# Kernel optimization log

Measured on AMD Instinct MI355X. Metric: run time of the kernel, lower is better.

The kernel has to match this reference:

```python
import jax, jax.numpy as jnp
import numpy as np

B, S, H = 8, 1024, 768
NH, DH = 12, 64
F, E = 3072, 8
EPS = 1e-12

def layer_norm(x, g, b):
    mu = jnp.mean(x, axis=-1, keepdims=True)
    var = jnp.var(x, axis=-1, keepdims=True)
    return g * (x - mu) / jnp.sqrt(var + EPS) + b

def setup_inputs():
    key = jax.random.key(0)
    ks = jax.random.split(key, 20)
    std = 0.02
    d = {
        'hidden_states': jax.random.normal(ks[0], (B, S, H), jnp.float32),
        'Wq': jax.random.normal(ks[1], (H, H)) * std, 'bq': jnp.zeros((H,)),
        'Wk': jax.random.normal(ks[2], (H, H)) * std, 'bk': jnp.zeros((H,)),
        'Wv': jax.random.normal(ks[3], (H, H)) * std, 'bv': jnp.zeros((H,)),
        'Wao': jax.random.normal(ks[4], (H, H)) * std, 'bao': jnp.zeros((H,)),
        'ln1_g': jnp.ones((H,)), 'ln1_b': jnp.zeros((H,)),
        'Wr': jax.random.normal(ks[5], (H, E)) * std, 'br': jnp.zeros((E,)),
        'Wi': jax.random.normal(ks[6], (E, H, F)) * std, 'bi': jnp.zeros((E, F)),
        'Wo': jax.random.normal(ks[7], (F, H)) * std, 'bo': jnp.zeros((H,)),
        'ln2_g': jnp.ones((H,)), 'ln2_b': jnp.zeros((H,)),
    }
    return d

def reference(hidden_states, Wq, bq, Wk, bk, Wv, bv, Wao, bao, ln1_g, ln1_b,
              Wr, br, Wi, bi, Wo, bo, ln2_g, ln2_b):
    b, s, h = hidden_states.shape
    # --- self attention ---
    q = (hidden_states @ Wq + bq).reshape(b, s, NH, DH)
    k = (hidden_states @ Wk + bk).reshape(b, s, NH, DH)
    v = (hidden_states @ Wv + bv).reshape(b, s, NH, DH)
    scores = jnp.einsum('bqhd,bkhd->bhqk', q, k) / jnp.sqrt(jnp.float32(DH))
    probs = jax.nn.softmax(scores, axis=-1)
    ctx = jnp.einsum('bhqk,bkhd->bqhd', probs, v).reshape(b, s, h)
    attention_output = layer_norm(ctx @ Wao + bao + hidden_states, ln1_g, ln1_b)
    # --- router ---
    routing_scores = jax.nn.softmax(attention_output @ Wr + br, axis=-1)  # [b,s,E]
    routing_expert = jnp.argmax(routing_scores, axis=-1)  # [b,s]
    # --- expert FFN (dispatch/combine via per-expert masking) ---
    flat_x = attention_output.reshape(-1, h)          # [T,H]
    flat_e = routing_expert.reshape(-1)               # [T]
    flat_inter = jnp.zeros((b * s, F), flat_x.dtype)
    for e in range(E):
        mask = (flat_e == e)[:, None].astype(flat_x.dtype)
        y = jax.nn.gelu(flat_x @ Wi[e] + bi[e], approximate=False)
        flat_inter = flat_inter + mask * y
    inter = flat_inter.reshape(b, s, F)
    # --- output (dense + residual layernorm) ---
    layer_output = layer_norm(inter @ Wo + bo + attention_output, ln2_g, ln2_b)
    return layer_output, routing_scores
```

## Files before the change

kernel.cpp:

```cpp
#include <hip/hip_runtime.h>
#include <math.h>
#include <stdint.h>

#define TOKS 8192
#define HDIM 768
#define FDIM 3072
#define NEXP 8
#define NHEAD 12
#define SEQ 1024
#define BATCH 8
#define PERMSZ 9216

typedef __attribute__((ext_vector_type(8))) short s16x8;
typedef __attribute__((ext_vector_type(4))) short s16x4;
typedef __attribute__((ext_vector_type(4))) float f32x4;

__device__ __forceinline__ short f2bf(float f) {
  uint32_t u = __float_as_uint(f);
  uint32_t r = (u + 0x7fffu + ((u >> 16) & 1u)) >> 16;
  return (short)(r & 0xffffu);
}
__device__ __forceinline__ float bf2f(short h) {
  return __uint_as_float(((uint32_t)(uint16_t)h) << 16);
}
__device__ __forceinline__ void gload16(const void* g, void* l) {
  __builtin_amdgcn_global_load_lds(
      (const __attribute__((address_space(1))) uint32_t*)g,
      (__attribute__((address_space(3))) uint32_t*)l, 16, 0, 0);
}
__device__ __forceinline__ void pipe_wait_barrier() {
  asm volatile("s_waitcnt vmcnt(0)" ::: "memory");
  __builtin_amdgcn_s_barrier();
}

__global__ __launch_bounds__(256) void convert_split(
    const float* __restrict__ X, short* __restrict__ Xh, short* __restrict__ Xl, int n4)
{
  const int i = blockIdx.x * 256 + threadIdx.x;
  if (i >= n4) return;
  const float4 v = ((const float4*)X)[i];
  const float a[4] = {v.x, v.y, v.z, v.w};
  s16x4 h, l;
#pragma unroll
  for (int j = 0; j < 4; ++j) {
    h[j] = f2bf(a[j]);
    l[j] = f2bf(a[j] - bf2f(h[j]));
  }
  ((s16x4*)Xh)[i] = h;
  ((s16x4*)Xl)[i] = l;
}

__global__ __launch_bounds__(256) void transpose_split(
    const float* __restrict__ W, short* __restrict__ WTh, short* __restrict__ WTl,
    int K, int N)
{
  __shared__ float t[32][33];
  const int tid = threadIdx.x;
  const int tx = tid & 31, ty = tid >> 5;
  const int n0 = blockIdx.x * 32, k0 = blockIdx.y * 32;
#pragma unroll
  for (int r = 0; r < 4; ++r)
    t[ty + r * 8][tx] = W[(size_t)(k0 + ty + r * 8) * N + n0 + tx];
  __syncthreads();
#pragma unroll
  for (int r = 0; r < 4; ++r) {
    const float v = t[tx][ty + r * 8];
    const short h = f2bf(v);
    WTh[(size_t)(n0 + ty + r * 8) * K + k0 + tx] = h;
    WTl[(size_t)(n0 + ty + r * 8) * K + k0 + tx] = f2bf(v - bf2f(h));
  }
}

__global__ __launch_bounds__(256) void qkv_split_mfma(
    const short* __restrict__ Ah, const short* __restrict__ Al,
    const short* __restrict__ BhT, const short* __restrict__ BlT,
    const float* __restrict__ bias,
    short* __restrict__ QKh, short* __restrict__ QKl,
    short* __restrict__ VTh, short* __restrict__ VTl)
{
  const int K = 768;
  __shared__ __align__(16) short lAh[4096];
  __shared__ __align__(16) short lAl[4096];
  __shared__ __align__(16) short lBh[2][4096];
  __shared__ __align__(16) short lBl[2][4096];
  const int dsp = blockIdx.x + 18 * blockIdx.y;
  const int orig = (dsp & 7) * 144 + (dsp >> 3);
  const int bx = orig % 18, by = orig / 18;
  const int tid = threadIdx.x;
  const int w = tid >> 6, lane = tid & 63;
  const int wr = w >> 1, wc = w & 1;
  const int row0 = by * 128, col0 = bx * 128;
  const int sr = lane & 15, kg = lane >> 4;
  const size_t a0 = (size_t)(row0 + 2 * w * 16 + sr) * K + kg * 8;
  const size_t a1 = a0 + (size_t)16 * K;
  const size_t b0 = (size_t)(col0 + 2 * w * 16 + sr) * K + kg * 8;
  const size_t b1 = b0 + (size_t)16 * K;
  const int d0 = (2 * w) * 512, d1 = (2 * w + 1) * 512;
#define STAGE_QA(k0) do { \
    gload16(Ah + a0 + (k0), &lAh[d0]); \
    gload16(Ah + a1 + (k0), &lAh[d1]); \
    gload16(Al + a0 + (k0), &lAl[d0]); \
    gload16(Al + a1 + (k0), &lAl[d1]); \
  } while (0)
#define STAGE_QB(bu, k0) do { \
    gload16(BhT + b0 + (k0), &lBh[bu][d0]); \
    gload16(BhT + b1 + (k0), &lBh[bu][d1]); \
    gload16(BlT + b0 + (k0), &lBl[bu][d0]); \
    gload16(BlT + b1 + (k0), &lBl[bu][d1]); \
  } while (0)
  f32x4 acc[4][4] = {};
  STAGE_QA(0);
  STAGE_QB(0, 0);
  pipe_wait_barrier();
  int cur = 0;
  for (int t = 0; t < 24; ++t) {
    s16x8 ah[4], al[4], bh[4], bl[4];
#pragma unroll
    for (int i = 0; i < 4; ++i) {
      ah[i] = *(const s16x8*)&lAh[(wr * 4 + i) * 512 + lane * 8];
      al[i] = *(const s16x8*)&lAl[(wr * 4 + i) * 512 + lane * 8];
      bh[i] = *(const s16x8*)&lBh[cur][(wc * 4 + i) * 512 + lane * 8];
      bl[i] = *(const s16x8*)&lBl[cur][(wc * 4 + i) * 512 + lane * 8];
    }
    __syncthreads();
    if (t < 23) {
      STAGE_QA((t + 1) * 32);
      STAGE_QB(cur ^ 1, (t + 1) * 32);
    }
#pragma unroll
    for (int mi = 0; mi < 4; ++mi)
#pragma unroll
      for (int ni = 0; ni < 4; ++ni) {
        acc[mi][ni] = __builtin_amdgcn_mfma_f32_16x16x32_bf16(ah[mi], bh[ni], acc[mi][ni], 0, 0, 0);
        acc[mi][ni] = __builtin_amdgcn_mfma_f32_16x16x32_bf16(ah[mi], bl[ni], acc[mi][ni], 0, 0, 0);
        acc[mi][ni] = __builtin_amdgcn_mfma_f32_16x16x32_bf16(al[mi], bh[ni], acc[mi][ni], 0, 0, 0);
      }
    pipe_wait_barrier();
    cur ^= 1;
  }
#undef STAGE_QA
#undef STAGE_QB
  const int cl = lane & 15, rg = lane >> 4;
#pragma unroll
  for (int mi = 0; mi < 4; ++mi)
#pragma unroll
    for (int ni = 0; ni < 4; ++ni) {
      const int c = col0 + wc * 64 + ni * 16 + cl;
      const int rowb = row0 + wr * 64 + mi * 16 + rg * 4;
      const float qscale = (c < 768) ? 0.125f : 1.0f;
      s16x4 hv, lv;
#pragma unroll
      for (int r = 0; r < 4; ++r) {
        const float v = (acc[mi][ni][r] + bias[c]) * qscale;
        const short hh = f2bf(v);
        hv[r] = hh;
        lv[r] = f2bf(v - bf2f(hh));
      }
      if (c < 1536) {
#pragma unroll
        for (int r = 0; r < 4; ++r) {
          QKh[(size_t)(rowb + r) * 1536 + c] = hv[r];
          QKl[(size_t)(rowb + r) * 1536 + c] = lv[r];
        }
      } else {
        const int dall = c - 1536;
        const size_t vi = (((size_t)((rowb >> 10) * NHEAD + (dall >> 6))) * 64 + (dall & 63)) * 1024
                          + (rowb & 1023);
        *(s16x4*)(VTh + vi) = hv;
        *(s16x4*)(VTl + vi) = lv;
      }
    }
}

__global__ __launch_bounds__(256) void gemm_splitk_staged(
    const short* __restrict__ Ah, const short* __restrict__ Al,
    const short* __restrict__ BhT, const short* __restrict__ BlT,
    const float* __restrict__ bias, float* __restrict__ C0, float* __restrict__ C1,
    int N, int K)
{
  __shared__ __align__(16) short lAh[2][4096];
  __shared__ __align__(16) short lAl[2][4096];
  __shared__ __align__(16) short lBh[2][4096];
  __shared__ __align__(16) short lBl[2][4096];
  const int tid = threadIdx.x;
  const int w = tid >> 6, lane = tid & 63;
  const int wr = w >> 1, wc = w & 1;
  const int row0 = blockIdx.y * 128, col0 = blockIdx.x * 128;
  const int z = blockIdx.z;
  const int Khalf = K >> 1, koff = z * Khalf;
  const int sr = lane & 15, kg = lane >> 4;
  const size_t a0 = (size_t)(row0 + 2 * w * 16 + sr) * K + koff + kg * 8;
  const size_t a1 = a0 + (size_t)16 * K;
  const size_t b0 = (size_t)(col0 + 2 * w * 16 + sr) * K + koff + kg * 8;
  const size_t b1 = b0 + (size_t)16 * K;
  const int d0 = (2 * w) * 512, d1 = (2 * w + 1) * 512;
#define STAGE_K4(bu, k0) do { \
    gload16(Ah + a0 + (k0), &lAh[bu][d0]); \
    gload16(Ah + a1 + (k0), &lAh[bu][d1]); \
    gload16(Al + a0 + (k0), &lAl[bu][d0]); \
    gload16(Al + a1 + (k0), &lAl[bu][d1]); \
    gload16(BhT + b0 + (k0), &lBh[bu][d0]); \
    gload16(BhT + b1 + (k0), &lBh[bu][d1]); \
    gload16(BlT + b0 + (k0), &lBl[bu][d0]); \
    gload16(BlT + b1 + (k0), &lBl[bu][d1]); \
  } while (0)
  f32x4 acc[4][4] = {};
  const int NT = Khalf >> 5;
  STAGE_K4(0, 0);
  pipe_wait_barrier();
  int cur = 0;
  for (int t = 0; t < NT; ++t) {
    if (t + 1 < NT) STAGE_K4(cur ^ 1, (t + 1) * 32);
    s16x8 ah[4], al[4], bh[4], bl[4];
#pragma unroll
    for (int i = 0; i < 4; ++i) {
      ah[i] = *(const s16x8*)&lAh[cur][(wr * 4 + i) * 512 + lane * 8];
      al[i] = *(const s16x8*)&lAl[cur][(wr * 4 + i) * 512 + lane * 8];
      bh[i] = *(const s16x8*)&lBh[cur][(wc * 4 + i) * 512 + lane * 8];
      bl[i] = *(const s16x8*)&lBl[cur][(wc * 4 + i) * 512 + lane * 8];
    }
#pragma unroll
    for (int mi = 0; mi < 4; ++mi)
#pragma unroll
      for (int ni = 0; ni < 4; ++ni) {
        acc[mi][ni] = __builtin_amdgcn_mfma_f32_16x16x32_bf16(ah[mi], bh[ni], acc[mi][ni], 0, 0, 0);
        acc[mi][ni] = __builtin_amdgcn_mfma_f32_16x16x32_bf16(ah[mi], bl[ni], acc[mi][ni], 0, 0, 0);
        acc[mi][ni] = __builtin_amdgcn_mfma_f32_16x16x32_bf16(al[mi], bh[ni], acc[mi][ni], 0, 0, 0);
      }
    pipe_wait_barrier();
    cur ^= 1;
  }
#undef STAGE_K4
  float* C = z ? C1 : C0;
  const int cl = lane & 15, rg = lane >> 4;
#pragma unroll
  for (int mi = 0; mi < 4; ++mi)
#pragma unroll
    for (int r = 0; r < 4; ++r) {
      const int row = row0 + wr * 64 + mi * 16 + rg * 4 + r;
#pragma unroll
      for (int ni = 0; ni < 4; ++ni) {
        const int c = col0 + wc * 64 + ni * 16 + cl;
        C[(size_t)row * N + c] = acc[mi][ni][r] + (z ? 0.f : bias[c]);
      }
    }
}

__global__ __launch_bounds__(128, 2) void attention_part(
    const short* __restrict__ QKh, const short* __restrict__ QKl,
    const short* __restrict__ VTh, const short* __restrict__ VTl,
    float* __restrict__ O0, float* __restrict__ O1,
    float2* __restrict__ ml0, float2* __restrict__ ml1)
{
  __shared__ __align__(16) short lPh[2][2560];
  const int tid = threadIdx.x;
  const int w = tid >> 6, lane = tid & 63;
  const int dsp = blockIdx.x + 32 * (blockIdx.y + 12 * blockIdx.z);
  const int orig = (dsp & 7) * 384 + (dsp >> 3);
  const int wx = orig & 31;
  const int b = orig / 384, h = (orig >> 5) % 12;
  const int z = wx & 1;
  const int q0 = (wx >> 1) * 64 + w * 32;
  const int kv0 = z * 512;
  const int sr = lane & 15, kg = lane >> 4;
  const int cl = sr, rg = kg;
  short* myPh = lPh[w];
  float* Op = z ? O1 : O0;
  float2* mlp = z ? ml1 : ml0;

  s16x8 qh[2][2], ql[2][2];
  {
    const size_t qbase = ((size_t)b * SEQ + q0 + sr) * 1536 + h * 64 + kg * 8;
#pragma unroll
    for (int mi = 0; mi < 2; ++mi)
#pragma unroll
      for (int ks = 0; ks < 2; ++ks) {
        const size_t o = qbase + (size_t)mi * (16 * 1536) + ks * 32;
        qh[mi][ks] = *(const s16x8*)(QKh + o);
        ql[mi][ks] = *(const s16x8*)(QKl + o);
      }
  }
  float m_run[2][4], l_run[2][4];
#pragma unroll
  for (int mi = 0; mi < 2; ++mi)
#pragma unroll
    for (int r = 0; r < 4; ++r) { m_run[mi][r] = -3.0e38f; l_run[mi][r] = 0.f; }
  f32x4 acc_o[2][4] = {};

  for (int kt = kv0; kt < kv0 + 512; kt += 64) {
    s16x8 kh[4][2], kl2[4][2];
    {
      const size_t kbase = ((size_t)b * SEQ + kt + sr) * 1536 + 768 + h * 64 + kg * 8;
#pragma unroll
      for (int ni = 0; ni < 4; ++ni)
#pragma unroll
        for (int ks = 0; ks < 2; ++ks) {
          const size_t o = kbase + (size_t)ni * (16 * 1536) + ks * 32;
          kh[ni][ks] = *(const s16x8*)(QKh + o);
          kl2[ni][ks] = *(const s16x8*)(QKl + o);
        }
    }
    f32x4 accs[2][4] = {};
    __builtin_amdgcn_s_setprio(1);
#pragma unroll
    for (int ks = 0; ks < 2; ++ks)
#pragma unroll
      for (int ni = 0; ni < 4; ++ni)
#pragma unroll
        for (int mi = 0; mi < 2; ++mi) {
          accs[mi][ni] = __builtin_amdgcn_mfma_f32_16x16x32_bf16(qh[mi][ks], kh[ni][ks], accs[mi][ni], 0, 0, 0);
          accs[mi][ni] = __builtin_amdgcn_mfma_f32_16x16x32_bf16(qh[mi][ks], kl2[ni][ks], accs[mi][ni], 0, 0, 0);
          accs[mi][ni] = __builtin_amdgcn_mfma_f32_16x16x32_bf16(ql[mi][ks], kh[ni][ks], accs[mi][ni], 0, 0, 0);
        }
    __builtin_amdgcn_s_setprio(0);
    s16x8 vh[4][2], vl2[4][2];
    {
      const size_t vbase = (((size_t)(b * NHEAD + h)) * 64 + sr) * 1024 + kt + kg * 8;
#pragma unroll
      for (int nd = 0; nd < 4; ++nd)
#pragma unroll
        for (int ks2 = 0; ks2 < 2; ++ks2) {
          const size_t o = vbase + (size_t)nd * (16 * 1024) + ks2 * 32;
          vh[nd][ks2] = *(const s16x8*)(VTh + o);
          vl2[nd][ks2] = *(const s16x8*)(VTl + o);
        }
    }
#pragma unroll
    for (int mi = 0; mi < 2; ++mi)
#pragma unroll
      for (int r = 0; r < 4; ++r) {
        float mx = fmaxf(fmaxf(accs[mi][0][r], accs[mi][1][r]),
                         fmaxf(accs[mi][2][r], accs[mi][3][r]));
        mx = fmaxf(mx, __shfl_xor(mx, 1));
        mx = fmaxf(mx, __shfl_xor(mx, 2));
        mx = fmaxf(mx, __shfl_xor(mx, 4));
        mx = fmaxf(mx, __shfl_xor(mx, 8));
        const float mn = fmaxf(m_run[mi][r], mx);
        const float c = __expf(m_run[mi][r] - mn);
        m_run[mi][r] = mn;
        l_run[mi][r] *= c;
#pragma unroll
        for (int nd = 0; nd < 4; ++nd) acc_o[mi][nd][r] *= c;
        float sum = 0.f;
#pragma unroll
        for (int ni = 0; ni < 4; ++ni) {
          const float p = __expf(accs[mi][ni][r] - mn);
          const short hh = f2bf(p);
          sum += bf2f(hh);
          const int idx = (mi * 2 + (ni >> 1)) * 640 + (rg * 4 + r) * 40 + (ni & 1) * 16 + cl;
          myPh[idx] = hh;
        }
        sum += __shfl_xor(sum, 1);
        sum += __shfl_xor(sum, 2);
        sum += __shfl_xor(sum, 4);
        sum += __shfl_xor(sum, 8);
        l_run[mi][r] += sum;
      }
    __builtin_amdgcn_s_setprio(1);
#pragma unroll
    for (int ks2 = 0; ks2 < 2; ++ks2) {
      s16x8 pf[2];
#pragma unroll
      for (int mi = 0; mi < 2; ++mi) {
        const int ra = (mi * 2 + ks2) * 640 + sr * 40 + kg * 8;
        pf[mi] = *(const s16x8*)&myPh[ra];
      }
#pragma unroll
      for (int nd = 0; nd < 4; ++nd)
#pragma unroll
        for (int mi = 0; mi < 2; ++mi) {
          acc_o[mi][nd] = __builtin_amdgcn_mfma_f32_16x16x32_bf16(pf[mi], vh[nd][ks2], acc_o[mi][nd], 0, 0, 0);
          acc_o[mi][nd] = __builtin_amdgcn_mfma_f32_16x16x32_bf16(pf[mi], vl2[nd][ks2], acc_o[mi][nd], 0, 0, 0);
        }
    }
    __builtin_amdgcn_s_setprio(0);
  }
#pragma unroll
  for (int mi = 0; mi < 2; ++mi)
#pragma unroll
    for (int nd = 0; nd < 4; ++nd)
#pragma unroll
      for (int r = 0; r < 4; ++r) {
        const int row = q0 + mi * 16 + rg * 4 + r;
        const int d = h * 64 + nd * 16 + cl;
        Op[((size_t)b * SEQ + row) * HDIM + d] = acc_o[mi][nd][r];
      }
  if (sr == 0) {
#pragma unroll
    for (int mi = 0; mi < 2; ++mi)
#pragma unroll
      for (int r = 0; r < 4; ++r) {
        const int row = q0 + mi * 16 + rg * 4 + r;
        mlp[(size_t)(b * NHEAD + h) * SEQ + row] = make_float2(m_run[mi][r], l_run[mi][r]);
      }
  }
}

__global__ __launch_bounds__(256) void combine_split(
    const float* __restrict__ O0, const float* __restrict__ O1,
    const float2* __restrict__ ml0, const float2* __restrict__ ml1,
    short* __restrict__ Ch, short* __restrict__ Cl)
{
  const int t = blockIdx.x;
  const int b = t >> 10, s = t & 1023;
  const int tid = threadIdx.x;
#pragma unroll
  for (int i = 0; i < 3; ++i) {
    const int idx = tid + i * 256;
    const int h = idx >> 6;
    const float2 a0 = ml0[(size_t)(b * NHEAD + h) * SEQ + s];
    const float2 a1 = ml1[(size_t)(b * NHEAD + h) * SEQ + s];
    const float mm = fmaxf(a0.x, a1.x);
    const float w0 = __expf(a0.x - mm), w1 = __expf(a1.x - mm);
    const float denom = a0.y * w0 + a1.y * w1;
    const size_t o = (size_t)t * HDIM + idx;
    const float v = (O0[o] * w0 + O1[o] * w1) / denom;
    const short hh = f2bf(v);
    Ch[o] = hh;
    Cl[o] = f2bf(v - bf2f(hh));
  }
}

__global__ __launch_bounds__(256) void transpose_to_bf16(
    const float* __restrict__ W, short* __restrict__ WT, int K, int N)
{
  const size_t off = (size_t)blockIdx.z * (size_t)K * N;
  const float* Wp = W + off;
  short* WTp = WT + off;
  __shared__ float t[32][33];
  const int tid = threadIdx.x;
  const int tx = tid & 31, ty = tid >> 5;
  const int n0 = blockIdx.x * 32, k0 = blockIdx.y * 32;
#pragma unroll
  for (int r = 0; r < 4; ++r)
    t[ty + r * 8][tx] = Wp[(size_t)(k0 + ty + r * 8) * N + n0 + tx];
  __syncthreads();
#pragma unroll
  for (int r = 0; r < 4; ++r)
    WTp[(size_t)(n0 + ty + r * 8) * K + k0 + tx] = f2bf(t[tx][ty + r * 8]);
}

__global__ __launch_bounds__(256) void expert_up_mfma(
    const short* __restrict__ Abf, const short* __restrict__ WiT,
    const float* __restrict__ bi, const int* __restrict__ perm,
    const int* __restrict__ offs, short* __restrict__ interb)
{
  const int row0 = blockIdx.x * 128;
  if (row0 >= offs[NEXP]) return;
  int e = 0;
  while (offs[e + 1] <= row0) ++e;
  __shared__ __align__(16) short lA[2][4096];
  __shared__ __align__(16) short lB[2][4096];
  __shared__ int toks[128];
  const int tid = threadIdx.x;
  const int w = tid >> 6, lane = tid & 63;
  const int wr = w >> 1, wc = w & 1;
  const int col0 = blockIdx.y * 128;
  if (tid < 128) toks[tid] = perm[row0 + tid];
  __syncthreads();
  const int sr = lane & 15, kg = lane >> 4;
  int t0 = toks[2 * w * 16 + sr];        if (t0 < 0) t0 = toks[0];
  int t1 = toks[(2 * w + 1) * 16 + sr];  if (t1 < 0) t1 = toks[0];
  const size_t a0 = (size_t)t0 * HDIM + kg * 8;
  const size_t a1 = (size_t)t1 * HDIM + kg * 8;
  const short* Bt = WiT + (size_t)e * FDIM * HDIM;
  const size_t b0 = (size_t)(col0 + 2 * w * 16 + sr) * HDIM + kg * 8;
  const size_t b1 = b0 + (size_t)16 * HDIM;
  const int d0 = (2 * w) * 512, d1 = (2 * w + 1) * 512;
#define STAGE_E(bu, k0) do { \
    gload16(Abf + a0 + (k0), &lA[bu][d0]); \
    gload16(Abf + a1 + (k0), &lA[bu][d1]); \
    gload16(Bt + b0 + (k0), &lB[bu][d0]); \
    gload16(Bt + b1 + (k0), &lB[bu][d1]); \
  } while (0)
  f32x4 acc[4][4] = {};
  STAGE_E(0, 0);
  pipe_wait_barrier();
  int cur = 0;
  for (int t = 0; t < 24; ++t) {
    if (t < 23) STAGE_E(cur ^ 1, (t + 1) * 32);
    s16x8 af[4], bg[4];
#pragma unroll
    for (int i = 0; i < 4; ++i) {
      af[i] = *(const s16x8*)&lA[cur][(wr * 4 + i) * 512 + lane * 8];
      bg[i] = *(const s16x8*)&lB[cur][(wc * 4 + i) * 512 + lane * 8];
    }
#pragma unroll
    for (int mi = 0; mi < 4; ++mi)
#pragma unroll
      for (int ni = 0; ni < 4; ++ni)
        acc[mi][ni] = __builtin_amdgcn_mfma_f32_16x16x32_bf16(af[mi], bg[ni], acc[mi][ni], 0, 0, 0);
    pipe_wait_barrier();
    cur ^= 1;
  }
#undef STAGE_E
  const int cl = lane & 15, rg = lane >> 4;
#pragma unroll
  for (int mi = 0; mi < 4; ++mi) {
#pragma unroll
    for (int r = 0; r < 4; ++r) {
      const int rl = wr * 64 + mi * 16 + rg * 4 + r;
      const int tok = toks[rl];
      if (tok < 0) continue;
#pragma unroll
      for (int ni = 0; ni < 4; ++ni) {
        const int c = col0 + wc * 64 + ni * 16 + cl;
        float v = acc[mi][ni][r] + bi[(size_t)e * FDIM + c];
        v = 0.5f * v * (1.0f + erff(v * 0.70710678118654752f));
        interb[(size_t)tok * FDIM + c] = f2bf(v);
      }
    }
  }
}

__global__ __launch_bounds__(256) void wo_mfma(
    const short* __restrict__ Ab, const short* __restrict__ BT,
    const float* __restrict__ bias, float* __restrict__ C0, float* __restrict__ C1)
{
  __shared__ __align__(16) short lA[2][4096];
  __shared__ __align__(16) short lB[2][4096];
  const int tid = threadIdx.x;
  const int w = tid >> 6, lane = tid & 63;
  const int wr = w >> 1, wc = w & 1;
  const int row0 = blockIdx.y * 128, col0 = blockIdx.x * 128;
  const int z = blockIdx.z;
  const int kbase = z * 1536;
  const int sr = lane & 15, kg = lane >> 4;
  const size_t a0 = (size_t)(row0 + 2 * w * 16 + sr) * FDIM + kbase + kg * 8;
  const size_t a1 = a0 + (size_t)16 * FDIM;
  const size_t b0 = (size_t)(col0 + 2 * w * 16 + sr) * FDIM + kbase + kg * 8;
  const size_t b1 = b0 + (size_t)16 * FDIM;
  const int d0 = (2 * w) * 512, d1 = (2 * w + 1) * 512;
#define STAGE_W(bu, k0) do { \
    gload16(Ab + a0 + (k0), &lA[bu][d0]); \
    gload16(Ab + a1 + (k0), &lA[bu][d1]); \
    gload16(BT + b0 + (k0), &lB[bu][d0]); \
    gload16(BT + b1 + (k0), &lB[bu][d1]); \
  } while (0)
  f32x4 acc[4][4] = {};
  STAGE_W(0, 0);
  pipe_wait_barrier();
  int cur = 0;
  for (int t = 0; t < 48; ++t) {
    if (t < 47) STAGE_W(cur ^ 1, (t + 1) * 32);
    s16x8 af[4], bg[4];
#pragma unroll
    for (int i = 0; i < 4; ++i) {
      af[i] = *(const s16x8*)&lA[cur][(wr * 4 + i) * 512 + lane * 8];
      bg[i] = *(const s16x8*)&lB[cur][(wc * 4 + i) * 512 + lane * 8];
    }
#pragma unroll
    for (int mi = 0; mi < 4; ++mi)
#pragma unroll
      for (int ni = 0; ni < 4; ++ni)
        acc[mi][ni] = __builtin_amdgcn_mfma_f32_16x16x32_bf16(af[mi], bg[ni], acc[mi][ni], 0, 0, 0);
    pipe_wait_barrier();
    cur ^= 1;
  }
#undef STAGE_W
  float* C = z ? C1 : C0;
  const int cl = lane & 15, rg = lane >> 4;
#pragma unroll
  for (int mi = 0; mi < 4; ++mi) {
#pragma unroll
    for (int r = 0; r < 4; ++r) {
      const int row = row0 + wr * 64 + mi * 16 + rg * 4 + r;
#pragma unroll
      for (int ni = 0; ni < 4; ++ni) {
        const int c = col0 + wc * 64 + ni * 16 + cl;
        C[(size_t)row * HDIM + c] = acc[mi][ni][r] + (z ? 0.f : bias[c]);
      }
    }
  }
}

__global__ __launch_bounds__(256) void add2_ln_kernel(
    const float* __restrict__ X1, const float* __restrict__ X2,
    const float* __restrict__ R, const float* __restrict__ g,
    const float* __restrict__ bb, float* __restrict__ out)
{
  const int t = blockIdx.x;
  const int tid = threadIdx.x;
  const float* x1 = X1 + (size_t)t * HDIM;
  const float* x2 = X2 + (size_t)t * HDIM;
  const float* r = R + (size_t)t * HDIM;
  float v[3];
  float sum = 0.f, ssq = 0.f;
#pragma unroll
  for (int i = 0; i < 3; ++i) {
    const float val = x1[tid + i * 256] + x2[tid + i * 256] + r[tid + i * 256];
    v[i] = val;
    sum += val;
    ssq += val * val;
  }
#pragma unroll
  for (int o = 32; o > 0; o >>= 1) {
    sum += __shfl_down(sum, o);
    ssq += __shfl_down(ssq, o);
  }
  __shared__ float red[10];
  const int wid = tid >> 6, lane = tid & 63;
  if (lane == 0) { red[wid] = sum; red[4 + wid] = ssq; }
  __syncthreads();
  if (tid == 0) {
    const float s = red[0] + red[1] + red[2] + red[3];
    const float q = red[4] + red[5] + red[6] + red[7];
    const float mean = s * (1.f / HDIM);
    const float var = q * (1.f / HDIM) - mean * mean;
    red[8] = mean;
    red[9] = rsqrtf(fmaxf(var, 0.f) + 1e-12f);
  }
  __syncthreads();
  const float mean = red[8], rstd = red[9];
#pragma unroll
  for (int i = 0; i < 3; ++i) {
    const int idx = tid + i * 256;
    out[(size_t)t * HDIM + idx] = g[idx] * (v[i] - mean) * rstd + bb[idx];
  }
}

__global__ __launch_bounds__(256) void add2_ln_bf16_kernel(
    const float* __restrict__ X1, const float* __restrict__ X2,
    const float* __restrict__ R, const float* __restrict__ g,
    const float* __restrict__ bb, float* __restrict__ out, short* __restrict__ outb)
{
  const int t = blockIdx.x;
  const int tid = threadIdx.x;
  const float* x1 = X1 + (size_t)t * HDIM;
  const float* x2 = X2 + (size_t)t * HDIM;
  const float* r = R + (size_t)t * HDIM;
  float v[3];
  float sum = 0.f, ssq = 0.f;
#pragma unroll
  for (int i = 0; i < 3; ++i) {
    const float val = x1[tid + i * 256] + x2[tid + i * 256] + r[tid + i * 256];
    v[i] = val;
    sum += val;
    ssq += val * val;
  }
#pragma unroll
  for (int o = 32; o > 0; o >>= 1) {
    sum += __shfl_down(sum, o);
    ssq += __shfl_down(ssq, o);
  }
  __shared__ float red[10];
  const int wid = tid >> 6, lane = tid & 63;
  if (lane == 0) { red[wid] = sum; red[4 + wid] = ssq; }
  __syncthreads();
  if (tid == 0) {
    const float s = red[0] + red[1] + red[2] + red[3];
    const float q = red[4] + red[5] + red[6] + red[7];
    const float mean = s * (1.f / HDIM);
    const float var = q * (1.f / HDIM) - mean * mean;
    red[8] = mean;
    red[9] = rsqrtf(fmaxf(var, 0.f) + 1e-12f);
  }
  __syncthreads();
  const float mean = red[8], rstd = red[9];
#pragma unroll
  for (int i = 0; i < 3; ++i) {
    const int idx = tid + i * 256;
    const float o = g[idx] * (v[i] - mean) * rstd + bb[idx];
    out[(size_t)t * HDIM + idx] = o;
    outb[(size_t)t * HDIM + idx] = f2bf(o);
  }
}

__global__ __launch_bounds__(256) void router_kernel(
    const float* __restrict__ X, const float* __restrict__ Wr,
    const float* __restrict__ br, float* __restrict__ scores_out,
    int* __restrict__ expert, int* __restrict__ counts)
{
  const int wid = threadIdx.x >> 6, lane = threadIdx.x & 63;
  const int tok = blockIdx.x * 4 + wid;
  const float* x = X + (size_t)tok * HDIM;
  float acc[8] = {};
  for (int k0 = 0; k0 < HDIM; k0 += 64) {
    const float xv = x[k0 + lane];
    const float* wrow = Wr + (size_t)(k0 + lane) * NEXP;
    const float4 w0 = *reinterpret_cast<const float4*>(wrow);
    const float4 w1 = *reinterpret_cast<const float4*>(wrow + 4);
    acc[0] = fmaf(xv, w0.x, acc[0]);
    acc[1] = fmaf(xv, w0.y, acc[1]);
    acc[2] = fmaf(xv, w0.z, acc[2]);
    acc[3] = fmaf(xv, w0.w, acc[3]);
    acc[4] = fmaf(xv, w1.x, acc[4]);
    acc[5] = fmaf(xv, w1.y, acc[5]);
    acc[6] = fmaf(xv, w1.z, acc[6]);
    acc[7] = fmaf(xv, w1.w, acc[7]);
  }
#pragma unroll
  for (int e = 0; e < 8; ++e)
#pragma unroll
    for (int o = 32; o > 0; o >>= 1) acc[e] += __shfl_down(acc[e], o);
  if (lane == 0) {
    float mx = -3.0e38f;
#pragma unroll
    for (int e = 0; e < 8; ++e) { acc[e] += br[e]; mx = fmaxf(mx, acc[e]); }
    float sum = 0.f;
#pragma unroll
    for (int e = 0; e < 8; ++e) { acc[e] = expf(acc[e] - mx); sum += acc[e]; }
    const float inv = 1.f / sum;
    int best = 0;
    float bv = acc[0];
#pragma unroll
    for (int e = 0; e < 8; ++e) {
      const float p = acc[e] * inv;
      scores_out[(size_t)tok * NEXP + e] = p;
      if (acc[e] > bv) { bv = acc[e]; best = e; }
    }
    expert[tok] = best;
    atomicAdd(&counts[best], 1);
  }
}

__global__ void offsets_kernel(const int* __restrict__ counts, int* __restrict__ offs)
{
  if (threadIdx.x == 0 && blockIdx.x == 0) {
    int a = 0;
    for (int e = 0; e < NEXP; ++e) {
      offs[e] = a;
      a += ((counts[e] + 127) >> 7) << 7;
    }
    offs[NEXP] = a;
  }
}

__global__ __launch_bounds__(256) void scatter_kernel(
    const int* __restrict__ expert, const int* __restrict__ offs,
    int* __restrict__ cursor, int* __restrict__ perm)
{
  const int t = blockIdx.x * 256 + threadIdx.x;
  if (t >= TOKS) return;
  const int e = expert[t];
  const int pos = atomicAdd(&cursor[e], 1);
  perm[offs[e] + pos] = t;
}

extern "C" void kernel_launch(void* const* d_in, const int* in_sizes, int n_in,
                              void* d_out, int out_size, void* d_ws, size_t ws_size,
                              hipStream_t stream) {
  const float* hidden = (const float*)d_in[0];
  const float* Wq  = (const float*)d_in[1];
  const float* bq  = (const float*)d_in[2];
  const float* Wk  = (const float*)d_in[3];
  const float* bk  = (const float*)d_in[4];
  const float* Wv  = (const float*)d_in[5];
  const float* bv  = (const float*)d_in[6];
  const float* Wao = (const float*)d_in[7];
  const float* bao = (const float*)d_in[8];
  const float* ln1g = (const float*)d_in[9];
  const float* ln1b = (const float*)d_in[10];
  const float* Wr  = (const float*)d_in[11];
  const float* br  = (const float*)d_in[12];
  const float* Wi  = (const float*)d_in[13];
  const float* bi  = (const float*)d_in[14];
  const float* Wo  = (const float*)d_in[15];
  const float* bo  = (const float*)d_in[16];
  const float* ln2g = (const float*)d_in[17];
  const float* ln2b = (const float*)d_in[18];

  float* out = (float*)d_out;
  float* scores_out = out + (size_t)TOKS * HDIM;

  const size_t M1 = (size_t)TOKS * HDIM;
  const size_t HW = (size_t)HDIM * HDIM;
  float* ws = (float*)d_ws;
  short* QKhb = (short*)ws;
  short* QKlb = (short*)(ws + M1);
  short* VThb = (short*)(ws + 2 * M1);
  short* VTlb = VThb + (size_t)BATCH * NHEAD * 64 * 1024;
  float* O0b  = ws + 3 * M1;
  float* O1b  = ws + 4 * M1;
  float* bqkv = ws + 3 * M1;
  short* Hh = (short*)(ws + 4 * M1);
  short* Hl = Hh + M1;
  short* Ch = (short*)(ws + 2 * M1);
  short* Cl = Ch + M1;
  short* wt = (short*)(ws + 5 * M1);
  short* WqkvhT = wt;
  short* WqkvlT = wt + 3 * HW;
  short* WaohT  = wt + 6 * HW;
  short* WaolT  = wt + 7 * HW;
  float2* ml0 = (float2*)(ws + 5 * M1 + 4 * HW);
  float2* ml1 = ml0 + (size_t)BATCH * NHEAD * SEQ;
  float* aoproj0  = ws;
  float* aoproj1  = ws + 3 * M1;
  float* attn_out = ws + M1;
  float* tmp2a    = ws;
  float* tmp2b    = ws + 3 * M1;
  short* Abf    = (short*)(ws + 2 * M1);
  short* WiT    = Abf + M1;
  short* WoT    = WiT + (size_t)NEXP * FDIM * HDIM;
  short* interb = WoT + (size_t)HDIM * FDIM;
  int* ints   = (int*)(interb + (size_t)TOKS * FDIM);
  int* perm   = ints;
  int* expert = ints + PERMSZ;
  int* counts = expert + TOKS;
  int* offs   = counts + NEXP;
  int* cursor = offs + NEXP + 1;

  hipMemsetAsync(counts, 0, (NEXP + NEXP + 1 + NEXP) * sizeof(int), stream);
  hipMemsetAsync(perm, 0xFF, PERMSZ * sizeof(int), stream);
  hipMemcpyAsync(bqkv,        bq, HDIM * sizeof(float), hipMemcpyDeviceToDevice, stream);
  hipMemcpyAsync(bqkv + 768,  bk, HDIM * sizeof(float), hipMemcpyDeviceToDevice, stream);
  hipMemcpyAsync(bqkv + 1536, bv, HDIM * sizeof(float), hipMemcpyDeviceToDevice, stream);

  const dim3 blk(256);
  convert_split<<<dim3(TOKS * HDIM / 4 / 256), blk, 0, stream>>>(hidden, Hh, Hl, TOKS * HDIM / 4);
  transpose_split<<<dim3(24, 24), blk, 0, stream>>>(Wq,  WqkvhT,          WqkvlT,          HDIM, HDIM);
  transpose_split<<<dim3(24, 24), blk, 0, stream>>>(Wk,  WqkvhT + HW,     WqkvlT + HW,     HDIM, HDIM);
  transpose_split<<<dim3(24, 24), blk, 0, stream>>>(Wv,  WqkvhT + 2 * HW, WqkvlT + 2 * HW, HDIM, HDIM);
  transpose_split<<<dim3(24, 24), blk, 0, stream>>>(Wao, WaohT,           WaolT,           HDIM, HDIM);

  qkv_split_mfma<<<dim3(2304 / 128, TOKS / 128), blk, 0, stream>>>(
      Hh, Hl, WqkvhT, WqkvlT, bqkv, QKhb, QKlb, VThb, VTlb);

  attention_part<<<dim3((SEQ / 64) * 2, NHEAD, BATCH), dim3(128), 0, stream>>>(
      QKhb, QKlb, VThb, VTlb, O0b, O1b, ml0, ml1);
  combine_split<<<dim3(TOKS), blk, 0, stream>>>(O0b, O1b, ml0, ml1, Ch, Cl);

  gemm_splitk_staged<<<dim3(HDIM / 128, TOKS / 128, 2), blk, 0, stream>>>(
      Ch, Cl, WaohT, WaolT, bao, aoproj0, aoproj1, HDIM, HDIM);
  add2_ln_bf16_kernel<<<dim3(TOKS), blk, 0, stream>>>(
      aoproj0, aoproj1, hidden, ln1g, ln1b, attn_out, Abf);

  router_kernel<<<dim3(TOKS / 4), blk, 0, stream>>>(attn_out, Wr, br, scores_out, expert, counts);
  offsets_kernel<<<dim3(1), dim3(64), 0, stream>>>(counts, offs);
  scatter_kernel<<<dim3(TOKS / 256), blk, 0, stream>>>(expert, offs, cursor, perm);

  transpose_to_bf16<<<dim3(FDIM / 32, HDIM / 32, NEXP), blk, 0, stream>>>(Wi, WiT, HDIM, FDIM);
  transpose_to_bf16<<<dim3(HDIM / 32, FDIM / 32, 1), blk, 0, stream>>>(Wo, WoT, FDIM, HDIM);

  expert_up_mfma<<<dim3(PERMSZ / 128, FDIM / 128), blk, 0, stream>>>(
      Abf, WiT, bi, perm, offs, interb);
  wo_mfma<<<dim3(HDIM / 128, TOKS / 128, 2), blk, 0, stream>>>(interb, WoT, bo, tmp2a, tmp2b);
  add2_ln_kernel<<<dim3(TOKS), blk, 0, stream>>>(tmp2a, tmp2b, attn_out, ln2g, ln2b, out);
}
```

Baseline: 865.0 us.

## Double attention query tile per wave and stream K/V fragments per k-slice

Each wave now handles 64 query rows instead of 32, with the block covering 128 queries and the grid halved. Every K/V fragment loaded from global memory is therefore reused across twice as many query rows. K and V loads are also split per k-slice, with the second V half loaded after the softmax, to hold down the register growth from the larger accumulators. The cost is higher register pressure and fewer blocks, which may reduce occupancy under launch_bounds(128,2).

```diff
diff --git a/kernel.cpp b/kernel.cpp
--- a/kernel.cpp
+++ b/kernel.cpp
@@ -252,15 +252,15 @@
     float* __restrict__ O0, float* __restrict__ O1,
     float2* __restrict__ ml0, float2* __restrict__ ml1)
 {
-  __shared__ __align__(16) short lPh[2][2560];
+  __shared__ __align__(16) short lPh[2][5120];
   const int tid = threadIdx.x;
   const int w = tid >> 6, lane = tid & 63;
-  const int dsp = blockIdx.x + 32 * (blockIdx.y + 12 * blockIdx.z);
-  const int orig = (dsp & 7) * 384 + (dsp >> 3);
-  const int wx = orig & 31;
-  const int b = orig / 384, h = (orig >> 5) % 12;
+  const int dsp = blockIdx.x + 16 * (blockIdx.y + 12 * blockIdx.z);
+  const int orig = (dsp & 7) * 192 + (dsp >> 3);
+  const int wx = orig & 15;
+  const int b = orig / 192, h = (orig >> 4) % 12;
   const int z = wx & 1;
-  const int q0 = (wx >> 1) * 64 + w * 32;
+  const int q0 = (wx >> 1) * 128 + w * 64;
   const int kv0 = z * 512;
   const int sr = lane & 15, kg = lane >> 4;
   const int cl = sr, rg = kg;
@@ -268,11 +268,11 @@
   float* Op = z ? O1 : O0;
   float2* mlp = z ? ml1 : ml0;
 
-  s16x8 qh[2][2], ql[2][2];
+  s16x8 qh[4][2], ql[4][2];
   {
     const size_t qbase = ((size_t)b * SEQ + q0 + sr) * 1536 + h * 64 + kg * 8;
 #pragma unroll
-    for (int mi = 0; mi < 2; ++mi)
+    for (int mi = 0; mi < 4; ++mi)
 #pragma unroll
       for (int ks = 0; ks < 2; ++ks) {
         const size_t o = qbase + (size_t)mi * (16 * 1536) + ks * 32;
@@ -280,53 +280,50 @@
         ql[mi][ks] = *(const s16x8*)(QKl + o);
       }
   }
-  float m_run[2][4], l_run[2][4];
-#pragma unroll
-  for (int mi = 0; mi < 2; ++mi)
+  float m_run[4][4], l_run[4][4];
+#pragma unroll
+  for (int mi = 0; mi < 4; ++mi)
 #pragma unroll
     for (int r = 0; r < 4; ++r) { m_run[mi][r] = -3.0e38f; l_run[mi][r] = 0.f; }
-  f32x4 acc_o[2][4] = {};
+  f32x4 acc_o[4][4] = {};
 
   for (int kt = kv0; kt < kv0 + 512; kt += 64) {
-    s16x8 kh[4][2], kl2[4][2];
-    {
-      const size_t kbase = ((size_t)b * SEQ + kt + sr) * 1536 + 768 + h * 64 + kg * 8;
+    f32x4 accs[4][4] = {};
+#pragma unroll
+    for (int ks = 0; ks < 2; ++ks) {
+      s16x8 kh[4], kl2[4];
+      {
+        const size_t kbase = ((size_t)b * SEQ + kt + sr) * 1536 + 768 + h * 64 + kg * 8 + ks * 32;
+#pragma unroll
+        for (int ni = 0; ni < 4; ++ni) {
+          const size_t o = kbase + (size_t)ni * (16 * 1536);
+          kh[ni] = *(const s16x8*)(QKh + o);
+          kl2[ni] = *(const s16x8*)(QKl + o);
+        }
+      }
+      __builtin_amdgcn_s_setprio(1);
 #pragma unroll
       for (int ni = 0; ni < 4; ++ni)
 #pragma unroll
-        for (int ks = 0; ks < 2; ++ks) {
-          const size_t o = kbase + (size_t)ni * (16 * 1536) + ks * 32;
-          kh[ni][ks] = *(const s16x8*)(QKh + o);
-          kl2[ni][ks] = *(const s16x8*)(QKl + o);
+        for (int mi = 0; mi < 4; ++mi) {
+          accs[mi][ni] = __builtin_amdgcn_mfma_f32_16x16x32_bf16(qh[mi][ks], kh[ni], accs[mi][ni], 0, 0, 0);
+          accs[mi][ni] = __builtin_amdgcn_mfma_f32_16x16x32_bf16(qh[mi][ks], kl2[ni], accs[mi][ni], 0, 0, 0);
+          accs[mi][ni] = __builtin_amdgcn_mfma_f32_16x16x32_bf16(ql[mi][ks], kh[ni], accs[mi][ni], 0, 0, 0);
         }
-    }
-    f32x4 accs[2][4] = {};
-    __builtin_amdgcn_s_setprio(1);
-#pragma unroll
-    for (int ks = 0; ks < 2; ++ks)
-#pragma unroll
-      for (int ni = 0; ni < 4; ++ni)
-#pragma unroll
-        for (int mi = 0; mi < 2; ++mi) {
-          accs[mi][ni] = __builtin_amdgcn_mfma_f32_16x16x32_bf16(qh[mi][ks], kh[ni][ks], accs[mi][ni], 0, 0, 0);
-          accs[mi][ni] = __builtin_amdgcn_mfma_f32_16x16x32_bf16(qh[mi][ks], kl2[ni][ks], accs[mi][ni], 0, 0, 0);
-          accs[mi][ni] = __builtin_amdgcn_mfma_f32_16x16x32_bf16(ql[mi][ks], kh[ni][ks], accs[mi][ni], 0, 0, 0);
-        }
-    __builtin_amdgcn_s_setprio(0);
-    s16x8 vh[4][2], vl2[4][2];
+      __builtin_amdgcn_s_setprio(0);
+    }
+    s16x8 vh0[4], vl0[4];
     {
       const size_t vbase = (((size_t)(b * NHEAD + h)) * 64 + sr) * 1024 + kt + kg * 8;
 #pragma unroll
-      for (int nd = 0; nd < 4; ++nd)
-#pragma unroll
-        for (int ks2 = 0; ks2 < 2; ++ks2) {
-          const size_t o = vbase + (size_t)nd * (16 * 1024) + ks2 * 32;
-          vh[nd][ks2] = *(const s16x8*)(VTh + o);
-          vl2[nd][ks2] = *(const s16x8*)(VTl + o);
-        }
-    }
-#pragma unroll
-    for (int mi = 0; mi < 2; ++mi)
+      for (int nd = 0; nd < 4; ++nd) {
+        const size_t o = vbase + (size_t)nd * (16 * 1024);
+        vh0[nd] = *(const s16x8*)(VTh + o);
+        vl0[nd] = *(const s16x8*)(VTl + o);
+      }
+    }
+#pragma unroll
+    for (int mi = 0; mi < 4; ++mi)
 #pragma unroll
       for (int r = 0; r < 4; ++r) {
         float mx = fmaxf(fmaxf(accs[mi][0][r], accs[mi][1][r]),
@@ -356,27 +353,47 @@
         sum += __shfl_xor(sum, 8);
         l_run[mi][r] += sum;
       }
+    s16x8 vh1[4], vl1[4];
+    {
+      const size_t vbase = (((size_t)(b * NHEAD + h)) * 64 + sr) * 1024 + kt + kg * 8 + 32;
+#pragma unroll
+      for (int nd = 0; nd < 4; ++nd) {
+        const size_t o = vbase + (size_t)nd * (16 * 1024);
+        vh1[nd] = *(const s16x8*)(VTh + o);
+        vl1[nd] = *(const s16x8*)(VTl + o);
+      }
+    }
     __builtin_amdgcn_s_setprio(1);
-#pragma unroll
-    for (int ks2 = 0; ks2 < 2; ++ks2) {
-      s16x8 pf[2];
-#pragma unroll
-      for (int mi = 0; mi < 2; ++mi) {
-        const int ra = (mi * 2 + ks2) * 640 + sr * 40 + kg * 8;
-        pf[mi] = *(const s16x8*)&myPh[ra];
-      }
+    {
+      s16x8 pf[4];
+#pragma unroll
+      for (int mi = 0; mi < 4; ++mi)
+        pf[mi] = *(const s16x8*)&myPh[(mi * 2 + 0) * 640 + sr * 40 + kg * 8];
 #pragma unroll
       for (int nd = 0; nd < 4; ++nd)
 #pragma unroll
-        for (int mi = 0; mi < 2; ++mi) {
-          acc_o[mi][nd] = __builtin_amdgcn_mfma_f32_16x16x32_bf16(pf[mi], vh[nd][ks2], acc_o[mi][nd], 0, 0, 0);
-          acc_o[mi][nd] = __builtin_amdgcn_mfma_f32_16x16x32_bf16(pf[mi], vl2[nd][ks2], acc_o[mi][nd], 0, 0, 0);
+        for (int mi = 0; mi < 4; ++mi) {
+          acc_o[mi][nd] = __builtin_amdgcn_mfma_f32_16x16x32_bf16(pf[mi], vh0[nd], acc_o[mi][nd], 0, 0, 0);
+          acc_o[mi][nd] = __builtin_amdgcn_mfma_f32_16x16x32_bf16(pf[mi], vl0[nd], acc_o[mi][nd], 0, 0, 0);
         }
     }
+    {
+      s16x8 pf[4];
+#pragma unroll
+      for (int mi = 0; mi < 4; ++mi)
+        pf[mi] = *(const s16x8*)&myPh[(mi * 2 + 1) * 640 + sr * 40 + kg * 8];
+#pragma unroll
+      for (int nd = 0; nd < 4; ++nd)
+#pragma unroll
+        for (int mi = 0; mi < 4; ++mi) {
+          acc_o[mi][nd] = __builtin_amdgcn_mfma_f32_16x16x32_bf16(pf[mi], vh1[nd], acc_o[mi][nd], 0, 0, 0);
+          acc_o[mi][nd] = __builtin_amdgcn_mfma_f32_16x16x32_bf16(pf[mi], vl1[nd], acc_o[mi][nd], 0, 0, 0);
+        }
+    }
     __builtin_amdgcn_s_setprio(0);
   }
 #pragma unroll
-  for (int mi = 0; mi < 2; ++mi)
+  for (int mi = 0; mi < 4; ++mi)
 #pragma unroll
     for (int nd = 0; nd < 4; ++nd)
 #pragma unroll
@@ -387,7 +404,7 @@
       }
   if (sr == 0) {
 #pragma unroll
-    for (int mi = 0; mi < 2; ++mi)
+    for (int mi = 0; mi < 4; ++mi)
 #pragma unroll
       for (int r = 0; r < 4; ++r) {
         const int row = q0 + mi * 16 + rg * 4 + r;
@@ -816,7 +833,7 @@
   qkv_split_mfma<<<dim3(2304 / 128, TOKS / 128), blk, 0, stream>>>(
       Hh, Hl, WqkvhT, WqkvlT, bqkv, QKhb, QKlb, VThb, VTlb);
 
-  attention_part<<<dim3((SEQ / 64) * 2, NHEAD, BATCH), dim3(128), 0, stream>>>(
+  attention_part<<<dim3((SEQ / 128) * 2, NHEAD, BATCH), dim3(128), 0, stream>>>(
       QKhb, QKlb, VThb, VTlb, O0b, O1b, ml0, ml1);
   combine_split<<<dim3(TOKS), blk, 0, stream>>>(O0b, O1b, ml0, ml1, Ch, Cl);
 
```

Result: no change. 868.2 us (+0.4%).
